# Kernel tuning notes

Hardware: AMD Instinct MI355X
Metric: run time of the kernel (lower is better)

## Reference

```python
import jax, jax.numpy as jnp
import numpy as np
from jax import lax

B, S, I, H, L = 128, 512, 128, 256, 2


def setup_inputs() -> dict:
    key = jax.random.key(0)
    ks = jax.random.split(key, 9)
    s_in = 1.0 / np.sqrt(I)
    s_h = 1.0 / np.sqrt(2 * H)
    return {
        "x": jax.random.normal(ks[0], (B, S, I), dtype=jnp.float32),
        "W_in": jax.random.normal(ks[1], (I, H), dtype=jnp.float32) * s_in,
        "b_in": jax.random.normal(ks[2], (H,), dtype=jnp.float32) * s_in,
        "Wz": jax.random.normal(ks[3], (L, 2 * H, H), dtype=jnp.float32) * s_h,
        "bz": jax.random.normal(ks[4], (L, H), dtype=jnp.float32) * s_h,
        "Wr": jax.random.normal(ks[5], (L, 2 * H, H), dtype=jnp.float32) * s_h,
        "br": jax.random.normal(ks[6], (L, H), dtype=jnp.float32) * s_h,
        "Wn": jax.random.normal(ks[7], (L, 2 * H, H), dtype=jnp.float32) * s_h,
        "bn": jax.random.normal(ks[8], (L, H), dtype=jnp.float32) * s_h,
    }


def reference(x, W_in, b_in, Wz, bz, Wr, br, Wn, bn):
    # x: [B, S, I] -> project to hidden once (matches self.input_layer(x))
    xp = jnp.einsum("bsi,ih->bsh", x, W_in) + b_in  # [B, S, H]
    n_layers = Wz.shape[0]
    b = x.shape[0]
    h0 = jnp.zeros((n_layers, b, H), dtype=x.dtype)

    def step(h, x_t):
        # h: [L, B, H], x_t: [B, H]
        inp = x_t
        h_next = []
        for l in range(n_layers):
            h_prev = h[l]
            comb = jnp.concatenate([inp, h_prev], axis=-1)  # [B, 2H]
            z = jax.nn.sigmoid(comb @ Wz[l] + bz[l])
            r = jax.nn.sigmoid(comb @ Wr[l] + br[l])
            comb2 = jnp.concatenate([inp, r * h_prev], axis=-1)
            n = jnp.tanh(comb2 @ Wn[l] + bn[l])
            hn = (1.0 - z) * n + z * h_prev
            h_next.append(hn)
            inp = hn
        h_new = jnp.stack(h_next)  # [L, B, H]
        return h_new, h_new[-1]

    h_final, outs = lax.scan(step, h0, jnp.swapaxes(xp, 0, 1))  # outs: [S, B, H]
    outputs = jnp.swapaxes(outs, 0, 1)  # [B, S, H]
    return outputs, h_final
```

## Files before the change

### kernel.cpp

```cpp
#include <hip/hip_runtime.h>
#include <stdint.h>

#define B_ 128
#define S_ 512
#define I_ 128
#define H_ 256

typedef short bf16x8 __attribute__((ext_vector_type(8)));
typedef short bf16x4 __attribute__((ext_vector_type(4)));
typedef float f32x4  __attribute__((ext_vector_type(4)));

__device__ __forceinline__ short f2bf(float f){
  unsigned u = __float_as_uint(f);
  u = (u + 0x7FFFu + ((u >> 16) & 1u)) >> 16;
  return (short)u;
}
__device__ __forceinline__ float bf2f(unsigned short u){
  return __uint_as_float(((unsigned)u) << 16);
}
__device__ __forceinline__ float sigmoidf_(float x){
  float e = __expf(-x);
  return __fdividef(1.f, 1.f + e);
}
__device__ __forceinline__ float tanhf_(float x){
  x = fminf(fmaxf(x, -10.f), 10.f);
  float e = __expf(2.f * x);
  return __fdividef(e - 1.f, e + 1.f);
}
__device__ __forceinline__ void bar_lds(){
  asm volatile("s_waitcnt lgkmcnt(0)" ::: "memory");
  __builtin_amdgcn_s_barrier();
}

#define MF(A, B, C) __builtin_amdgcn_mfma_f32_16x16x32_bf16((A), (B), (C), 0, 0, 0)

__global__ __launch_bounds__(256) void prep_compute(
    const float* __restrict__ W_in, const float* __restrict__ b_in,
    const float* __restrict__ Wz, const float* __restrict__ bz,
    const float* __restrict__ Wr, const float* __restrict__ br,
    const float* __restrict__ Wn, const float* __restrict__ bn,
    float* __restrict__ WcT, float* __restrict__ bc, float* __restrict__ bcat1)
{
  int id = blockIdx.x * 256 + threadIdx.x;
  if (id < 98304){
    int i = id / 768, gcol = id % 768;
    int g = gcol >> 8, n = gcol & 255;
    const float* Wg = (g == 0) ? Wz : (g == 1) ? Wr : Wn;
    float s = 0.f;
    for (int j = 0; j < 256; j++) s += W_in[i * 256 + j] * Wg[j * 256 + n];
    WcT[i * 768 + gcol] = s;
  } else if (id < 99072){
    int gcol = id - 98304;
    int g = gcol >> 8, n = gcol & 255;
    const float* Wg = (g == 0) ? Wz : (g == 1) ? Wr : Wn;
    const float* bg = (g == 0) ? bz : (g == 1) ? br : bn;
    float s = 0.f;
    for (int j = 0; j < 256; j++) s += b_in[j] * Wg[j * 256 + n];
    bc[gcol] = s + bg[n];
  } else if (id < 99840){
    int gcol = id - 99072;
    int g = gcol >> 8, n = gcol & 255;
    const float* bg = (g == 0) ? bz : (g == 1) ? br : bn;
    bcat1[gcol] = bg[256 + n];
  }
}


__global__ __launch_bounds__(256) void pack_wc(short* __restrict__ dst, const float* __restrict__ WcT)
{
  int id = blockIdx.x * 256 + threadIdx.x;
  int j = id & 7, l = (id >> 3) & 63, kt = (id >> 9) & 3, nt = id >> 11;
  int k = kt * 32 + (l >> 4) * 8 + j;
  int gcol = nt * 16 + (l & 15);
  dst[id] = f2bf(WcT[k * 768 + gcol]);
}

__global__ __launch_bounds__(256) void pack_top(short* __restrict__ dst,
    const float* __restrict__ Wz, const float* __restrict__ Wr, const float* __restrict__ Wn)
{
  int id = blockIdx.x * 256 + threadIdx.x;
  int j = id & 7, l = (id >> 3) & 63, kt = (id >> 9) & 7, nt = id >> 12;
  int k = kt * 32 + (l >> 4) * 8 + j;
  int gcol = nt * 16 + (l & 15);
  int g = gcol >> 8, n = gcol & 255;
  const float* W = (g == 0) ? Wz : (g == 1) ? Wr : Wn;
  dst[id] = f2bf(W[(size_t)(512 + k) * 256 + n]);
}

__global__ __launch_bounds__(256) void pack_zr(short* __restrict__ dst,
    const float* __restrict__ Wz, const float* __restrict__ Wr, int layer)
{
  int id = blockIdx.x * 256 + threadIdx.x;
  int j = id & 7, l = (id >> 3) & 63, kt = (id >> 9) & 7, nt = id >> 12;
  int k = kt * 32 + (l >> 4) * 8 + j;
  int n = (nt & 15) * 16 + (l & 15);
  const float* W = (nt < 16) ? Wz : Wr;
  dst[id] = f2bf(W[((size_t)layer * 512 + 256 + k) * 256 + n]);
}

__global__ __launch_bounds__(256) void pack_n(short* __restrict__ dst,
    const float* __restrict__ Wn, int layer)
{
  int id = blockIdx.x * 256 + threadIdx.x;
  int j = id & 7, l = (id >> 3) & 63, kt = (id >> 9) & 7, nt = id >> 12;
  int k = kt * 32 + (l >> 4) * 8 + j;
  int n = nt * 16 + (l & 15);
  dst[id] = f2bf(Wn[((size_t)layer * 512 + 256 + k) * 256 + n]);
}

template<bool ABF16, int KT>
__global__ __launch_bounds__(256) void gemm_kernel(
    const void* __restrict__ Ap, const short* __restrict__ BF,
    const float* __restrict__ bias, short* __restrict__ C)
{
  const int tid = threadIdx.x, w = tid >> 6, l = tid & 63;
  const int m0 = blockIdx.x * 64 + w * 16;
  const int nb = blockIdx.y;
  const int K = KT * 32;
  f32x4 zero4 = {0.f, 0.f, 0.f, 0.f};
  f32x4 acc[8];
#pragma unroll
  for (int nt = 0; nt < 8; nt++) acc[nt] = zero4;

#pragma unroll
  for (int kt = 0; kt < KT; kt++){
    bf16x8 af;
    if (ABF16){
      af = *(const bf16x8*)((const short*)Ap + (size_t)(m0 + (l & 15)) * K + kt * 32 + (l >> 4) * 8);
    } else {
      const float* A = (const float*)Ap + (size_t)(m0 + (l & 15)) * K + kt * 32 + (l >> 4) * 8;
      f32x4 a0 = *(const f32x4*)A;
      f32x4 a1 = *(const f32x4*)(A + 4);
      af[0] = f2bf(a0[0]); af[1] = f2bf(a0[1]); af[2] = f2bf(a0[2]); af[3] = f2bf(a0[3]);
      af[4] = f2bf(a1[0]); af[5] = f2bf(a1[1]); af[6] = f2bf(a1[2]); af[7] = f2bf(a1[3]);
    }
#pragma unroll
    for (int nt = 0; nt < 8; nt++){
      bf16x8 bf = *(const bf16x8*)(BF + (size_t)(((nb * 8 + nt) * KT + kt) * 64 + l) * 8);
      acc[nt] = __builtin_amdgcn_mfma_f32_16x16x32_bf16(af, bf, acc[nt], 0, 0, 0);
    }
  }
#pragma unroll
  for (int nt = 0; nt < 8; nt++){
    int col = nb * 128 + nt * 16 + (l & 15);
    float bv = bias[col];
#pragma unroll
    for (int rr = 0; rr < 4; rr++){
      int mrow = m0 + (l >> 4) * 4 + rr;
      C[(size_t)mrow * 768 + col] = f2bf(acc[nt][rr] + bv);
    }
  }
}

__global__ __launch_bounds__(256) void repack6(const unsigned short* __restrict__ Gbuf,
                                               short* __restrict__ GpA4, unsigned* __restrict__ GpB2)
{
  int id = blockIdx.x * 256 + threadIdx.x;
  int cix = id & 15, wv = (id >> 4) & 7, t = (id >> 7) & 511, row = id >> 16;
  short v[6];
#pragma unroll
  for (int i = 0; i < 2; i++)
#pragma unroll
    for (int g = 0; g < 3; g++)
      v[i * 3 + g] =
        (short)Gbuf[((size_t)row * 512 + t) * 768 + g * 256 + i * 128 + wv * 16 + cix];
  bf16x4 a = {v[0], v[1], v[2], v[3]};
  *(bf16x4*)(GpA4 + (size_t)id * 4) = a;
  GpB2[id] = (unsigned)(unsigned short)v[4] | ((unsigned)(unsigned short)v[5] << 16);
}

template<bool OUT_BF16>
__global__ __launch_bounds__(512, 1) void recur_kernel(
    const short* __restrict__ GpA4, const unsigned* __restrict__ GpB2,
    const short* __restrict__ WzrF, const short* __restrict__ WnF,
    void* __restrict__ outp, float* __restrict__ finals)
{
  __shared__ __align__(16) char ldsb[4096];

  const int tid = threadIdx.x;
  const int w = tid >> 6, l = tid & 63;
  const int cix = l & 15, lk = l >> 4;
  const int r0 = blockIdx.x;
  const int chunkBase = blockIdx.x * 65536 + w * 16 + cix;

  *(uint64_t*)(ldsb + tid * 8) = 0ull;

  bf16x8 wzr[4][8];
  bf16x8 wn[2][8];
#pragma unroll
  for (int i = 0; i < 4; i++)
#pragma unroll
    for (int kt = 0; kt < 8; kt++)
      wzr[i][kt] = *(const bf16x8*)(WzrF + (size_t)((((w + 8 * i) * 8 + kt) * 64 + l) * 8));
#pragma unroll
  for (int i = 0; i < 2; i++)
#pragma unroll
    for (int kt = 0; kt < 8; kt++)
      wn[i][kt] = *(const bf16x8*)(WnF + (size_t)((((w + 8 * i) * 8 + kt) * 64 + l) * 8));
  __syncthreads();

  const int A0 = (cix == 0) ? (lk << 4) : 1024;
  const int col0 = w * 16 + cix, col1 = col0 + 128;
  const int oA00 = col0 * 2;
  const int oA10 = col1 * 2;

  float h00 = 0.f, h10 = 0.f;

  bf16x4 rgA0{}, rgA1{};
  unsigned rgB0 = 0, rgB1 = 0;
  if (lk == 0){
    rgA0 = *(const bf16x4*)(GpA4 + (size_t)chunkBase * 4);
    rgB0 = GpB2[chunkBase];
    rgA1 = *(const bf16x4*)(GpA4 + (size_t)(chunkBase + 128) * 4);
    rgB1 = GpB2[chunkBase + 128];
  }

  const f32x4 Z4 = {0.f, 0.f, 0.f, 0.f};

#define AF_ZR(KT) (*(const bf16x8*)(ldsb + A0 + (KT) * 64))
#define AF_N(KT)  (*(const bf16x8*)(ldsb + A0 + (KT) * 64 + 2048))

#define STEP(T, RGA, RGB) do { \
     \
    bf16x8 x0 = AF_ZR(0), x1 = AF_ZR(1), x2 = AF_ZR(2), x3 = AF_ZR(3); \
    f32x4 az0 = Z4, az1 = Z4, ar0 = Z4, ar1 = Z4; \
    __builtin_amdgcn_s_setprio(1); \
    az0 = MF(x0, wzr[0][0], az0); az1 = MF(x0, wzr[1][0], az1); \
    ar0 = MF(x0, wzr[2][0], ar0); ar1 = MF(x0, wzr[3][0], ar1); x0 = AF_ZR(4); \
    az0 = MF(x1, wzr[0][1], az0); az1 = MF(x1, wzr[1][1], az1); \
    ar0 = MF(x1, wzr[2][1], ar0); ar1 = MF(x1, wzr[3][1], ar1); x1 = AF_ZR(5); \
    az0 = MF(x2, wzr[0][2], az0); az1 = MF(x2, wzr[1][2], az1); \
    ar0 = MF(x2, wzr[2][2], ar0); ar1 = MF(x2, wzr[3][2], ar1); x2 = AF_ZR(6); \
    az0 = MF(x3, wzr[0][3], az0); az1 = MF(x3, wzr[1][3], az1); \
    ar0 = MF(x3, wzr[2][3], ar0); ar1 = MF(x3, wzr[3][3], ar1); x3 = AF_ZR(7); \
    az0 = MF(x0, wzr[0][4], az0); az1 = MF(x0, wzr[1][4], az1); \
    ar0 = MF(x0, wzr[2][4], ar0); ar1 = MF(x0, wzr[3][4], ar1); \
    az0 = MF(x1, wzr[0][5], az0); az1 = MF(x1, wzr[1][5], az1); \
    ar0 = MF(x1, wzr[2][5], ar0); ar1 = MF(x1, wzr[3][5], ar1); \
    az0 = MF(x2, wzr[0][6], az0); az1 = MF(x2, wzr[1][6], az1); \
    ar0 = MF(x2, wzr[2][6], ar0); ar1 = MF(x2, wzr[3][6], ar1); \
    az0 = MF(x3, wzr[0][7], az0); az1 = MF(x3, wzr[1][7], az1); \
    ar0 = MF(x3, wzr[2][7], ar0); ar1 = MF(x3, wzr[3][7], ar1); \
    __builtin_amdgcn_s_setprio(0); \
     \
    float gn00 = 0.f, gn10 = 0.f; \
    float zv00 = 0.f, zv10 = 0.f; \
    if (lk == 0){ \
      float gz00 = bf2f((unsigned short)RGA[0]), gr00 = bf2f((unsigned short)RGA[1]); \
      gn00 = bf2f((unsigned short)RGA[2]); \
      float gz10 = bf2f((unsigned short)RGA[3]); \
      float gr10 = bf2f((unsigned short)(RGB & 0xffffu)); \
      gn10 = bf2f((unsigned short)(RGB >> 16)); \
      int tn = (T) + 2; if (tn >= S_) tn = (T); \
      size_t ch = (size_t)chunkBase + (size_t)tn * 128; \
      RGA = *(const bf16x4*)(GpA4 + ch * 4); \
      RGB = GpB2[ch]; \
      zv00 = sigmoidf_(az0[0] + gz00); zv10 = sigmoidf_(az1[0] + gz10); \
      float rv00 = sigmoidf_(ar0[0] + gr00), rv10 = sigmoidf_(ar1[0] + gr10); \
      *(short*)(ldsb + 2048 + oA00) = f2bf(rv00 * h00); \
      *(short*)(ldsb + 2048 + oA10) = f2bf(rv10 * h10); \
    } \
    bar_lds(); \
     \
    bf16x8 y0 = AF_N(0), y1 = AF_N(1); \
    f32x4 an0 = Z4, an1 = Z4; \
    __builtin_amdgcn_s_setprio(1); \
    an0 = MF(y0, wn[0][0], an0); an1 = MF(y0, wn[1][0], an1); y0 = AF_N(2); \
    an0 = MF(y1, wn[0][1], an0); an1 = MF(y1, wn[1][1], an1); y1 = AF_N(3); \
    an0 = MF(y0, wn[0][2], an0); an1 = MF(y0, wn[1][2], an1); y0 = AF_N(4); \
    an0 = MF(y1, wn[0][3], an0); an1 = MF(y1, wn[1][3], an1); y1 = AF_N(5); \
    an0 = MF(y0, wn[0][4], an0); an1 = MF(y0, wn[1][4], an1); y0 = AF_N(6); \
    an0 = MF(y1, wn[0][5], an0); an1 = MF(y1, wn[1][5], an1); y1 = AF_N(7); \
    an0 = MF(y0, wn[0][6], an0); an1 = MF(y0, wn[1][6], an1); \
    an0 = MF(y1, wn[0][7], an0); an1 = MF(y1, wn[1][7], an1); \
    __builtin_amdgcn_s_setprio(0); \
     \
    if (lk == 0){ \
      float nv00 = tanhf_(an0[0] + gn00), nv10 = tanhf_(an1[0] + gn10); \
      h00 = (1.f - zv00) * nv00 + zv00 * h00; \
      h10 = (1.f - zv10) * nv10 + zv10 * h10; \
      *(short*)(ldsb + oA00) = f2bf(h00); \
      *(short*)(ldsb + oA10) = f2bf(h10); \
      size_t ob = ((size_t)r0 * S_ + (T)) * H_; \
      if (OUT_BF16){ \
        ((short*)outp)[ob + col0] = f2bf(h00); \
        ((short*)outp)[ob + col1] = f2bf(h10); \
      } else { \
        ((float*)outp)[ob + col0] = h00; \
        ((float*)outp)[ob + col1] = h10; \
      } \
    } \
    bar_lds(); \
  } while (0)

#pragma unroll 1
  for (int t = 0; t < S_; t += 2){
    STEP(t, rgA0, rgB0);
    STEP(t + 1, rgA1, rgB1);
  }
#undef STEP
#undef AF_ZR
#undef AF_N

  if (lk == 0){
    finals[(size_t)r0 * H_ + col0] = h00;
    finals[(size_t)r0 * H_ + col1] = h10;
  }
}

extern "C" void kernel_launch(void* const* d_in, const int* in_sizes, int n_in,
                              void* d_out, int out_size, void* d_ws, size_t ws_size,
                              hipStream_t stream)
{
  (void)in_sizes; (void)n_in; (void)out_size; (void)ws_size;
  const float* x    = (const float*)d_in[0];
  const float* W_in = (const float*)d_in[1];
  const float* b_in = (const float*)d_in[2];
  const float* Wz   = (const float*)d_in[3];
  const float* bz   = (const float*)d_in[4];
  const float* Wr   = (const float*)d_in[5];
  const float* br   = (const float*)d_in[6];
  const float* Wn   = (const float*)d_in[7];
  const float* bn   = (const float*)d_in[8];
  float* out = (float*)d_out;

  char* ws = (char*)d_ws;
  short*    Gbuf  = (short*)(ws + 0);
  short*    GpA4  = (short*)(ws + 100663296);
  unsigned* GpB2  = (unsigned*)(ws + 167772160);
  float* WcT   = (float*)(ws + 201326592);
  float* bc    = (float*)(ws + 201719808);
  float* bcat1 = (float*)(ws + 201722880);
  short* WCF   = (short*)(ws + 201725952);
  short* W1TF  = (short*)(ws + 201922560);
  short* WZR0  = (short*)(ws + 202315776);
  short* WN0   = (short*)(ws + 202577920);
  short* WZR1  = (short*)(ws + 202708992);
  short* WN1   = (short*)(ws + 202971136);
  short* pipe  = (short*)(ws + 203102208);

  prep_compute<<<390, 256, 0, stream>>>(W_in, b_in, Wz, bz, Wr, br, Wn, bn, WcT, bc, bcat1);
  pack_wc <<<384, 256, 0, stream>>>(WCF, WcT);
  pack_top<<<768, 256, 0, stream>>>(W1TF, Wz, Wr, Wn);
  pack_zr <<<512, 256, 0, stream>>>(WZR0, Wz, Wr, 0);
  pack_n  <<<256, 256, 0, stream>>>(WN0, Wn, 0);
  pack_zr <<<512, 256, 0, stream>>>(WZR1, Wz, Wr, 1);
  pack_n  <<<256, 256, 0, stream>>>(WN1, Wn, 1);

  gemm_kernel<false, 4><<<dim3(1024, 6), 256, 0, stream>>>(x, WCF, bc, Gbuf);
  repack6<<<32768, 256, 0, stream>>>((const unsigned short*)Gbuf, GpA4, GpB2);
  recur_kernel<true><<<B_, 512, 0, stream>>>(GpA4, GpB2, WZR0, WN0, pipe, out + 16777216);
  gemm_kernel<true, 8><<<dim3(1024, 6), 256, 0, stream>>>(pipe, W1TF, bcat1, Gbuf);
  repack6<<<32768, 256, 0, stream>>>((const unsigned short*)Gbuf, GpA4, GpB2);
  recur_kernel<false><<<B_, 512, 0, stream>>>(GpA4, GpB2, WZR1, WN1, out, out + 16777216 + 32768);
}
```

Before: 1.491 ms.

## Fuse both GRU layers into one wavefront-pipelined persistent kernel with flags

Layer 0 and layer 1 recurrences now run in one launch of 256 blocks. The first 128 blocks compute layer 0 and publish progress flags every 16 timesteps. The other 128 blocks wait on those flags, compute the layer-1 input projection for each 16-step chunk on the fly with MFMA, and then run the layer-1 recurrence. This removes the separate layer-1 GEMM, the repack and the serial second recurrence, so the two layers overlap in time. It depends on all 256 blocks being co-resident and on the spin-wait with acquire/release flags. It also uses large LDS for the staged Wn weights.

```diff
diff --git a/kernel.cpp b/kernel.cpp
--- a/kernel.cpp
+++ b/kernel.cpp
@@ -31,7 +31,6 @@
   asm volatile("s_waitcnt lgkmcnt(0)" ::: "memory");
   __builtin_amdgcn_s_barrier();
 }
-
 #define MF(A, B, C) __builtin_amdgcn_mfma_f32_16x16x32_bf16((A), (B), (C), 0, 0, 0)
 
 __global__ __launch_bounds__(256) void prep_compute(
@@ -65,7 +64,6 @@
   }
 }
 
-
 __global__ __launch_bounds__(256) void pack_wc(short* __restrict__ dst, const float* __restrict__ WcT)
 {
   int id = blockIdx.x * 256 + threadIdx.x;
@@ -108,36 +106,30 @@
   dst[id] = f2bf(Wn[((size_t)layer * 512 + 256 + k) * 256 + n]);
 }
 
-template<bool ABF16, int KT>
-__global__ __launch_bounds__(256) void gemm_kernel(
-    const void* __restrict__ Ap, const short* __restrict__ BF,
+__global__ __launch_bounds__(256) void gemm_g0(
+    const float* __restrict__ Ap, const short* __restrict__ BF,
     const float* __restrict__ bias, short* __restrict__ C)
 {
   const int tid = threadIdx.x, w = tid >> 6, l = tid & 63;
   const int m0 = blockIdx.x * 64 + w * 16;
   const int nb = blockIdx.y;
-  const int K = KT * 32;
+  const int K = 128;
   f32x4 zero4 = {0.f, 0.f, 0.f, 0.f};
   f32x4 acc[8];
 #pragma unroll
   for (int nt = 0; nt < 8; nt++) acc[nt] = zero4;
-
-#pragma unroll
-  for (int kt = 0; kt < KT; kt++){
+#pragma unroll
+  for (int kt = 0; kt < 4; kt++){
+    const float* A = Ap + (size_t)(m0 + (l & 15)) * K + kt * 32 + (l >> 4) * 8;
+    f32x4 a0 = *(const f32x4*)A;
+    f32x4 a1 = *(const f32x4*)(A + 4);
     bf16x8 af;
-    if (ABF16){
-      af = *(const bf16x8*)((const short*)Ap + (size_t)(m0 + (l & 15)) * K + kt * 32 + (l >> 4) * 8);
-    } else {
-      const float* A = (const float*)Ap + (size_t)(m0 + (l & 15)) * K + kt * 32 + (l >> 4) * 8;
-      f32x4 a0 = *(const f32x4*)A;
-      f32x4 a1 = *(const f32x4*)(A + 4);
-      af[0] = f2bf(a0[0]); af[1] = f2bf(a0[1]); af[2] = f2bf(a0[2]); af[3] = f2bf(a0[3]);
-      af[4] = f2bf(a1[0]); af[5] = f2bf(a1[1]); af[6] = f2bf(a1[2]); af[7] = f2bf(a1[3]);
-    }
+    af[0] = f2bf(a0[0]); af[1] = f2bf(a0[1]); af[2] = f2bf(a0[2]); af[3] = f2bf(a0[3]);
+    af[4] = f2bf(a1[0]); af[5] = f2bf(a1[1]); af[6] = f2bf(a1[2]); af[7] = f2bf(a1[3]);
 #pragma unroll
     for (int nt = 0; nt < 8; nt++){
-      bf16x8 bf = *(const bf16x8*)(BF + (size_t)(((nb * 8 + nt) * KT + kt) * 64 + l) * 8);
-      acc[nt] = __builtin_amdgcn_mfma_f32_16x16x32_bf16(af, bf, acc[nt], 0, 0, 0);
+      bf16x8 bf = *(const bf16x8*)(BF + (size_t)(((nb * 8 + nt) * 4 + kt) * 64 + l) * 8);
+      acc[nt] = MF(af, bf, acc[nt]);
     }
   }
 #pragma unroll
@@ -169,59 +161,59 @@
   GpB2[id] = (unsigned)(unsigned short)v[4] | ((unsigned)(unsigned short)v[5] << 16);
 }
 
-template<bool OUT_BF16>
-__global__ __launch_bounds__(512, 1) void recur_kernel(
+__global__ __launch_bounds__(512, 1) void fused_recur(
     const short* __restrict__ GpA4, const unsigned* __restrict__ GpB2,
-    const short* __restrict__ WzrF, const short* __restrict__ WnF,
-    void* __restrict__ outp, float* __restrict__ finals)
-{
-  __shared__ __align__(16) char ldsb[4096];
+    const short* __restrict__ WZR0F, const short* __restrict__ WN0F,
+    const short* __restrict__ WZR1F, const short* __restrict__ WN1F,
+    const short* __restrict__ W1TF, const float* __restrict__ bcat1,
+    short* __restrict__ pipe, float* __restrict__ out,
+    float* __restrict__ finals, unsigned* __restrict__ flags)
+{
+  __shared__ __align__(16) char  ldsb[4096];
+  __shared__ __align__(16) short wnL[65536];
+  __shared__ __align__(16) short p1L[12288];
 
   const int tid = threadIdx.x;
   const int w = tid >> 6, l = tid & 63;
   const int cix = l & 15, lk = l >> 4;
-  const int r0 = blockIdx.x;
-  const int chunkBase = blockIdx.x * 65536 + w * 16 + cix;
+  const f32x4 Z4 = {0.f, 0.f, 0.f, 0.f};
 
   *(uint64_t*)(ldsb + tid * 8) = 0ull;
-
-  bf16x8 wzr[4][8];
-  bf16x8 wn[2][8];
-#pragma unroll
-  for (int i = 0; i < 4; i++)
-#pragma unroll
-    for (int kt = 0; kt < 8; kt++)
-      wzr[i][kt] = *(const bf16x8*)(WzrF + (size_t)((((w + 8 * i) * 8 + kt) * 64 + l) * 8));
-#pragma unroll
-  for (int i = 0; i < 2; i++)
-#pragma unroll
-    for (int kt = 0; kt < 8; kt++)
-      wn[i][kt] = *(const bf16x8*)(WnF + (size_t)((((w + 8 * i) * 8 + kt) * 64 + l) * 8));
-  __syncthreads();
 
   const int A0 = (cix == 0) ? (lk << 4) : 1024;
   const int col0 = w * 16 + cix, col1 = col0 + 128;
-  const int oA00 = col0 * 2;
-  const int oA10 = col1 * 2;
-
+  const int oA00 = col0 * 2, oA10 = col1 * 2;
   float h00 = 0.f, h10 = 0.f;
-
-  bf16x4 rgA0{}, rgA1{};
-  unsigned rgB0 = 0, rgB1 = 0;
-  if (lk == 0){
-    rgA0 = *(const bf16x4*)(GpA4 + (size_t)chunkBase * 4);
-    rgB0 = GpB2[chunkBase];
-    rgA1 = *(const bf16x4*)(GpA4 + (size_t)(chunkBase + 128) * 4);
-    rgB1 = GpB2[chunkBase + 128];
-  }
-
-  const f32x4 Z4 = {0.f, 0.f, 0.f, 0.f};
 
 #define AF_ZR(KT) (*(const bf16x8*)(ldsb + A0 + (KT) * 64))
 #define AF_N(KT)  (*(const bf16x8*)(ldsb + A0 + (KT) * 64 + 2048))
 
-#define STEP(T, RGA, RGB) do { \
-     \
+  if (blockIdx.x < 128){
+    const int r0 = blockIdx.x;
+    const int chunkBase = blockIdx.x * 65536 + w * 16 + cix;
+    bf16x8 wzr[4][8], wn[2][8];
+#pragma unroll
+    for (int i = 0; i < 4; i++)
+#pragma unroll
+      for (int kt = 0; kt < 8; kt++)
+        wzr[i][kt] = *(const bf16x8*)(WZR0F + (size_t)((((w + 8 * i) * 8 + kt) * 64 + l) * 8));
+#pragma unroll
+    for (int i = 0; i < 2; i++)
+#pragma unroll
+      for (int kt = 0; kt < 8; kt++)
+        wn[i][kt] = *(const bf16x8*)(WN0F + (size_t)((((w + 8 * i) * 8 + kt) * 64 + l) * 8));
+    __syncthreads();
+
+    bf16x4 rgA0{}, rgA1{};
+    unsigned rgB0 = 0, rgB1 = 0;
+    if (lk == 0){
+      rgA0 = *(const bf16x4*)(GpA4 + (size_t)chunkBase * 4);
+      rgB0 = GpB2[chunkBase];
+      rgA1 = *(const bf16x4*)(GpA4 + (size_t)(chunkBase + 128) * 4);
+      rgB1 = GpB2[chunkBase + 128];
+    }
+
+#define STEP0(T, RGA, RGB) do { \
     bf16x8 x0 = AF_ZR(0), x1 = AF_ZR(1), x2 = AF_ZR(2), x3 = AF_ZR(3); \
     f32x4 az0 = Z4, az1 = Z4, ar0 = Z4, ar1 = Z4; \
     __builtin_amdgcn_s_setprio(1); \
@@ -242,9 +234,7 @@
     az0 = MF(x3, wzr[0][7], az0); az1 = MF(x3, wzr[1][7], az1); \
     ar0 = MF(x3, wzr[2][7], ar0); ar1 = MF(x3, wzr[3][7], ar1); \
     __builtin_amdgcn_s_setprio(0); \
-     \
-    float gn00 = 0.f, gn10 = 0.f; \
-    float zv00 = 0.f, zv10 = 0.f; \
+    float gn00 = 0.f, gn10 = 0.f, zv00 = 0.f, zv10 = 0.f; \
     if (lk == 0){ \
       float gz00 = bf2f((unsigned short)RGA[0]), gr00 = bf2f((unsigned short)RGA[1]); \
       gn00 = bf2f((unsigned short)RGA[2]); \
@@ -261,7 +251,6 @@
       *(short*)(ldsb + 2048 + oA10) = f2bf(rv10 * h10); \
     } \
     bar_lds(); \
-     \
     bf16x8 y0 = AF_N(0), y1 = AF_N(1); \
     f32x4 an0 = Z4, an1 = Z4; \
     __builtin_amdgcn_s_setprio(1); \
@@ -274,7 +263,6 @@
     an0 = MF(y0, wn[0][6], an0); an1 = MF(y0, wn[1][6], an1); \
     an0 = MF(y1, wn[0][7], an0); an1 = MF(y1, wn[1][7], an1); \
     __builtin_amdgcn_s_setprio(0); \
-     \
     if (lk == 0){ \
       float nv00 = tanhf_(an0[0] + gn00), nv10 = tanhf_(an1[0] + gn10); \
       h00 = (1.f - zv00) * nv00 + zv00 * h00; \
@@ -282,30 +270,193 @@
       *(short*)(ldsb + oA00) = f2bf(h00); \
       *(short*)(ldsb + oA10) = f2bf(h10); \
       size_t ob = ((size_t)r0 * S_ + (T)) * H_; \
-      if (OUT_BF16){ \
-        ((short*)outp)[ob + col0] = f2bf(h00); \
-        ((short*)outp)[ob + col1] = f2bf(h10); \
-      } else { \
-        ((float*)outp)[ob + col0] = h00; \
-        ((float*)outp)[ob + col1] = h10; \
-      } \
+      pipe[ob + col0] = f2bf(h00); \
+      pipe[ob + col1] = f2bf(h10); \
     } \
     bar_lds(); \
   } while (0)
 
 #pragma unroll 1
-  for (int t = 0; t < S_; t += 2){
-    STEP(t, rgA0, rgB0);
-    STEP(t + 1, rgA1, rgB1);
+    for (int t = 0; t < S_; t += 2){
+      STEP0(t, rgA0, rgB0);
+      STEP0(t + 1, rgA1, rgB1);
+      if ((t & 15) == 14){
+        __syncthreads();
+        if (tid == 0)
+          __hip_atomic_store(&flags[r0], (unsigned)((t + 2) >> 4),
+                             __ATOMIC_RELEASE, __HIP_MEMORY_SCOPE_AGENT);
+      }
+    }
+#undef STEP0
+    if (lk == 0){
+      finals[(size_t)r0 * H_ + col0] = h00;
+      finals[(size_t)r0 * H_ + col1] = h10;
+    }
+  } else {
+    const int b = blockIdx.x - 128;
+    bf16x8 wzr[4][8];
+#pragma unroll
+    for (int i = 0; i < 4; i++)
+#pragma unroll
+      for (int kt = 0; kt < 8; kt++)
+        wzr[i][kt] = *(const bf16x8*)(WZR1F + (size_t)((((w + 8 * i) * 8 + kt) * 64 + l) * 8));
+#pragma unroll
+    for (int i = 0; i < 2; i++)
+#pragma unroll
+      for (int kt = 0; kt < 8; kt++){
+        bf16x8 v = *(const bf16x8*)(WN1F + (size_t)((((w + 8 * i) * 8 + kt) * 64 + l) * 8));
+        *(bf16x8*)(wnL + (size_t)(((w * 2 + i) * 8 + kt) * 64 + l) * 8) = v;
+      }
+    __syncthreads();
+
+    const short* wn0p = wnL + (size_t)(w * 2 + 0) * 8 * 512 + l * 8;
+    const short* wn1p = wnL + (size_t)(w * 2 + 1) * 8 * 512 + l * 8;
+#define WNL0(KT)  (*(const bf16x8*)(wn0p + (KT) * 512))
+#define WNL1(KT)  (*(const bf16x8*)(wn1p + (KT) * 512))
+
+    const short* wt0 = W1TF + (size_t)(w)      * 8 * 512 + l * 8;
+    const short* wt1 = W1TF + (size_t)(16 + w) * 8 * 512 + l * 8;
+    const short* wt2 = W1TF + (size_t)(32 + w) * 8 * 512 + l * 8;
+    const short* wt3 = W1TF + (size_t)(8 + w)  * 8 * 512 + l * 8;
+    const short* wt4 = W1TF + (size_t)(24 + w) * 8 * 512 + l * 8;
+    const short* wt5 = W1TF + (size_t)(40 + w) * 8 * 512 + l * 8;
+    float bb0 = bcat1[0 * 256 + 0 + w * 16 + cix];
+    float bb1 = bcat1[1 * 256 + 0 + w * 16 + cix];
+    float bb2 = bcat1[2 * 256 + 0 + w * 16 + cix];
+    float bb3 = bcat1[0 * 256 + 128 + w * 16 + cix];
+    float bb4 = bcat1[1 * 256 + 128 + w * 16 + cix];
+    float bb5 = bcat1[2 * 256 + 128 + w * 16 + cix];
+    short* p1Lw = p1L + w * 1536;
+
+#pragma unroll 1
+    for (int c = 0; c < 32; c++){
+      if (tid == 0){
+        unsigned target = (unsigned)(c + 1);
+        int guard = 0;
+        while (__hip_atomic_load(&flags[b], __ATOMIC_ACQUIRE, __HIP_MEMORY_SCOPE_AGENT) < target){
+          __builtin_amdgcn_s_sleep(4);
+          if (++guard > (1 << 20)) break;
+        }
+      }
+      __syncthreads();
+
+      const short* hp = pipe + ((size_t)b * 512 + c * 16 + cix) * 256 + lk * 8;
+      f32x4 p0 = Z4, p1 = Z4, p2 = Z4, p3 = Z4, p4 = Z4, p5 = Z4;
+      bf16x8 a0 = *(const bf16x8*)(hp + 0 * 32), a1 = *(const bf16x8*)(hp + 1 * 32);
+      bf16x8 a2 = *(const bf16x8*)(hp + 2 * 32), a3 = *(const bf16x8*)(hp + 3 * 32);
+      bf16x8 b0 = *(const bf16x8*)(wt0), b1 = *(const bf16x8*)(wt1), b2 = *(const bf16x8*)(wt2);
+      bf16x8 b3 = *(const bf16x8*)(wt3), b4 = *(const bf16x8*)(wt4), b5 = *(const bf16x8*)(wt5);
+#define GKT(AX, KTN) \
+      p0 = MF(AX, b0, p0); b0 = *(const bf16x8*)(wt0 + (KTN) * 512); \
+      p1 = MF(AX, b1, p1); b1 = *(const bf16x8*)(wt1 + (KTN) * 512); \
+      p2 = MF(AX, b2, p2); b2 = *(const bf16x8*)(wt2 + (KTN) * 512); \
+      p3 = MF(AX, b3, p3); b3 = *(const bf16x8*)(wt3 + (KTN) * 512); \
+      p4 = MF(AX, b4, p4); b4 = *(const bf16x8*)(wt4 + (KTN) * 512); \
+      p5 = MF(AX, b5, p5); b5 = *(const bf16x8*)(wt5 + (KTN) * 512);
+#define GKTL(AX) \
+      p0 = MF(AX, b0, p0); p1 = MF(AX, b1, p1); p2 = MF(AX, b2, p2); \
+      p3 = MF(AX, b3, p3); p4 = MF(AX, b4, p4); p5 = MF(AX, b5, p5);
+      GKT(a0, 1); a0 = *(const bf16x8*)(hp + 4 * 32);
+      GKT(a1, 2); a1 = *(const bf16x8*)(hp + 5 * 32);
+      GKT(a2, 3); a2 = *(const bf16x8*)(hp + 6 * 32);
+      GKT(a3, 4); a3 = *(const bf16x8*)(hp + 7 * 32);
+      GKT(a0, 5);
+      GKT(a1, 6);
+      GKT(a2, 7);
+      GKTL(a3);
+#undef GKT
+#undef GKTL
+#pragma unroll
+      for (int r = 0; r < 4; r++){
+        int tl = lk * 4 + r;
+        int base = (tl * 16 + cix) * 6;
+        unsigned u0 = (unsigned)(unsigned short)f2bf(p0[r]) | ((unsigned)(unsigned short)f2bf(p1[r]) << 16);
+        unsigned u1 = (unsigned)(unsigned short)f2bf(p2[r]) | ((unsigned)(unsigned short)f2bf(p3[r]) << 16);
+        unsigned u2 = (unsigned)(unsigned short)f2bf(p4[r]) | ((unsigned)(unsigned short)f2bf(p5[r]) << 16);
+        *(unsigned*)(p1Lw + base)     = u0;
+        *(unsigned*)(p1Lw + base + 2) = u1;
+        *(unsigned*)(p1Lw + base + 4) = u2;
+      }
+
+#pragma unroll 1
+      for (int ts = 0; ts < 16; ts++){
+        int T = c * 16 + ts;
+        float gz00 = 0.f, gr00 = 0.f, gn00 = 0.f, gz10 = 0.f, gr10 = 0.f, gn10 = 0.f;
+        if (lk == 0){
+          const short* pb = p1Lw + (ts * 16 + cix) * 6;
+          unsigned u0 = *(const unsigned*)(pb);
+          unsigned u1 = *(const unsigned*)(pb + 2);
+          unsigned u2 = *(const unsigned*)(pb + 4);
+          gz00 = bf2f((unsigned short)(u0 & 0xffffu)) + bb0;
+          gr00 = bf2f((unsigned short)(u0 >> 16)) + bb1;
+          gn00 = bf2f((unsigned short)(u1 & 0xffffu)) + bb2;
+          gz10 = bf2f((unsigned short)(u1 >> 16)) + bb3;
+          gr10 = bf2f((unsigned short)(u2 & 0xffffu)) + bb4;
+          gn10 = bf2f((unsigned short)(u2 >> 16)) + bb5;
+        }
+        bf16x8 x0 = AF_ZR(0), x1 = AF_ZR(1), x2 = AF_ZR(2), x3 = AF_ZR(3);
+        f32x4 az0 = Z4, az1 = Z4, ar0 = Z4, ar1 = Z4;
+        __builtin_amdgcn_s_setprio(1);
+        az0 = MF(x0, wzr[0][0], az0); az1 = MF(x0, wzr[1][0], az1);
+        ar0 = MF(x0, wzr[2][0], ar0); ar1 = MF(x0, wzr[3][0], ar1); x0 = AF_ZR(4);
+        az0 = MF(x1, wzr[0][1], az0); az1 = MF(x1, wzr[1][1], az1);
+        ar0 = MF(x1, wzr[2][1], ar0); ar1 = MF(x1, wzr[3][1], ar1); x1 = AF_ZR(5);
+        az0 = MF(x2, wzr[0][2], az0); az1 = MF(x2, wzr[1][2], az1);
+        ar0 = MF(x2, wzr[2][2], ar0); ar1 = MF(x2, wzr[3][2], ar1); x2 = AF_ZR(6);
+        az0 = MF(x3, wzr[0][3], az0); az1 = MF(x3, wzr[1][3], az1);
+        ar0 = MF(x3, wzr[2][3], ar0); ar1 = MF(x3, wzr[3][3], ar1); x3 = AF_ZR(7);
+        az0 = MF(x0, wzr[0][4], az0); az1 = MF(x0, wzr[1][4], az1);
+        ar0 = MF(x0, wzr[2][4], ar0); ar1 = MF(x0, wzr[3][4], ar1);
+        az0 = MF(x1, wzr[0][5], az0); az1 = MF(x1, wzr[1][5], az1);
+        ar0 = MF(x1, wzr[2][5], ar0); ar1 = MF(x1, wzr[3][5], ar1);
+        az0 = MF(x2, wzr[0][6], az0); az1 = MF(x2, wzr[1][6], az1);
+        ar0 = MF(x2, wzr[2][6], ar0); ar1 = MF(x2, wzr[3][6], ar1);
+        az0 = MF(x3, wzr[0][7], az0); az1 = MF(x3, wzr[1][7], az1);
+        ar0 = MF(x3, wzr[2][7], ar0); ar1 = MF(x3, wzr[3][7], ar1);
+        __builtin_amdgcn_s_setprio(0);
+        float zv00 = 0.f, zv10 = 0.f;
+        if (lk == 0){
+          zv00 = sigmoidf_(az0[0] + gz00); zv10 = sigmoidf_(az1[0] + gz10);
+          float rv00 = sigmoidf_(ar0[0] + gr00), rv10 = sigmoidf_(ar1[0] + gr10);
+          *(short*)(ldsb + 2048 + oA00) = f2bf(rv00 * h00);
+          *(short*)(ldsb + 2048 + oA10) = f2bf(rv10 * h10);
+        }
+        bf16x8 w00 = WNL0(0), w10 = WNL1(0), w01 = WNL0(1), w11 = WNL1(1);
+        bar_lds();
+        bf16x8 y0 = AF_N(0), y1 = AF_N(1);
+        f32x4 an0 = Z4, an1 = Z4;
+        __builtin_amdgcn_s_setprio(1);
+        an0 = MF(y0, w00, an0); an1 = MF(y0, w10, an1); y0 = AF_N(2); w00 = WNL0(2); w10 = WNL1(2);
+        an0 = MF(y1, w01, an0); an1 = MF(y1, w11, an1); y1 = AF_N(3); w01 = WNL0(3); w11 = WNL1(3);
+        an0 = MF(y0, w00, an0); an1 = MF(y0, w10, an1); y0 = AF_N(4); w00 = WNL0(4); w10 = WNL1(4);
+        an0 = MF(y1, w01, an0); an1 = MF(y1, w11, an1); y1 = AF_N(5); w01 = WNL0(5); w11 = WNL1(5);
+        an0 = MF(y0, w00, an0); an1 = MF(y0, w10, an1); y0 = AF_N(6); w00 = WNL0(6); w10 = WNL1(6);
+        an0 = MF(y1, w01, an0); an1 = MF(y1, w11, an1); y1 = AF_N(7); w01 = WNL0(7); w11 = WNL1(7);
+        an0 = MF(y0, w00, an0); an1 = MF(y0, w10, an1);
+        an0 = MF(y1, w01, an0); an1 = MF(y1, w11, an1);
+        __builtin_amdgcn_s_setprio(0);
+        if (lk == 0){
+          float nv00 = tanhf_(an0[0] + gn00), nv10 = tanhf_(an1[0] + gn10);
+          h00 = (1.f - zv00) * nv00 + zv00 * h00;
+          h10 = (1.f - zv10) * nv10 + zv10 * h10;
+          *(short*)(ldsb + oA00) = f2bf(h00);
+          *(short*)(ldsb + oA10) = f2bf(h10);
+          size_t ob = ((size_t)b * S_ + T) * H_;
+          out[ob + col0] = h00;
+          out[ob + col1] = h10;
+        }
+        bar_lds();
+      }
+    }
+#undef WNL0
+#undef WNL1
+    if (lk == 0){
+      finals[32768 + (size_t)b * H_ + col0] = h00;
+      finals[32768 + (size_t)b * H_ + col1] = h10;
+    }
   }
-#undef STEP
 #undef AF_ZR
 #undef AF_N
-
-  if (lk == 0){
-    finals[(size_t)r0 * H_ + col0] = h00;
-    finals[(size_t)r0 * H_ + col1] = h10;
-  }
 }
 
 extern "C" void kernel_launch(void* const* d_in, const int* in_sizes, int n_in,
@@ -338,6 +489,7 @@
   short* WZR1  = (short*)(ws + 202708992);
   short* WN1   = (short*)(ws + 202971136);
   short* pipe  = (short*)(ws + 203102208);
+  unsigned* flags = (unsigned*)(ws + 236656640);
 
   prep_compute<<<390, 256, 0, stream>>>(W_in, b_in, Wz, bz, Wr, br, Wn, bn, WcT, bc, bcat1);
   pack_wc <<<384, 256, 0, stream>>>(WCF, WcT);
@@ -347,10 +499,9 @@
   pack_zr <<<512, 256, 0, stream>>>(WZR1, Wz, Wr, 1);
   pack_n  <<<256, 256, 0, stream>>>(WN1, Wn, 1);
 
-  gemm_kernel<false, 4><<<dim3(1024, 6), 256, 0, stream>>>(x, WCF, bc, Gbuf);
+  gemm_g0<<<dim3(1024, 6), 256, 0, stream>>>(x, WCF, bc, Gbuf);
   repack6<<<32768, 256, 0, stream>>>((const unsigned short*)Gbuf, GpA4, GpB2);
-  recur_kernel<true><<<B_, 512, 0, stream>>>(GpA4, GpB2, WZR0, WN0, pipe, out + 16777216);
-  gemm_kernel<true, 8><<<dim3(1024, 6), 256, 0, stream>>>(pipe, W1TF, bcat1, Gbuf);
-  repack6<<<32768, 256, 0, stream>>>((const unsigned short*)Gbuf, GpA4, GpB2);
-  recur_kernel<false><<<B_, 512, 0, stream>>>(GpA4, GpB2, WZR1, WN1, out, out + 16777216 + 32768);
-}
+  hipMemsetAsync(flags, 0, 128 * sizeof(unsigned), stream);
+  fused_recur<<<256, 512, 0, stream>>>(GpA4, GpB2, WZR0, WN0, WZR1, WN1, W1TF, bcat1,
+                                       pipe, out, out + 16777216, flags);
+}
```

New measurement: 1.297 ms (median of 2 runs). 13.0% less time.
